# Optimization experiments

Hardware: AMD Instinct MI355X
Metric: run time of the kernel (lower is better)

The kernel has to match this reference:

```python
import jax, jax.numpy as jnp
import numpy as np
import math

B, S = 2, 2048
IN_FEATURES = 4096
OUT_FEATURES = 4096
BLOCK_SIZE = 64
NUM_FFT_MATRICES = 4
IN_BLOCKS = IN_FEATURES // BLOCK_SIZE
OUT_BLOCKS = OUT_FEATURES // BLOCK_SIZE  # 64


def setup_inputs() -> dict:
    key = jax.random.key(0)
    k1, k2 = jax.random.split(key)
    scale = 1.0 / math.sqrt(BLOCK_SIZE * IN_BLOCKS)
    x = jax.random.normal(k1, (B, S, IN_FEATURES), dtype=jnp.float32)
    circulant_params = jax.random.normal(
        k2, (NUM_FFT_MATRICES, OUT_BLOCKS, IN_BLOCKS, BLOCK_SIZE), dtype=jnp.float32) * scale
    channel_weights = jnp.ones((NUM_FFT_MATRICES,), dtype=jnp.float32) / NUM_FFT_MATRICES
    return {"x": x, "circulant_params": circulant_params, "channel_weights": channel_weights}


def reference(x, circulant_params, channel_weights):
    b, s, in_feat = x.shape
    # split channels into circulant blocks: (b, s, in_blocks, block)
    x_blocks = x.reshape(b, s, IN_BLOCKS, BLOCK_SIZE)
    x_fft = jnp.fft.rfft(x_blocks, axis=-1)                    # (b, s, i, F) complex
    circ_fft = jnp.fft.rfft(circulant_params, axis=-1)         # (m, o, i, F) complex
    # channel-weighted combine over the m fft matrices (linear, so fold into weights)
    circ_w = jnp.einsum('m,moif->oif', channel_weights.astype(circ_fft.dtype), circ_fft)
    # per-frequency complex contraction over in_blocks (the block-circulant matmul)
    y_fft = jnp.einsum('bsif,oif->bsof', x_fft, circ_w)        # (b, s, o, F)
    y = jnp.fft.irfft(y_fft, n=BLOCK_SIZE, axis=-1)            # (b, s, o, block)
    return y.reshape(b, s, OUT_FEATURES).astype(x.dtype)
```

## Files before the change

kernel.cpp:

```cpp
#include <hip/hip_runtime.h>
#include <math.h>


typedef unsigned short u16;
typedef unsigned int   u32;
typedef __attribute__((ext_vector_type(8))) short bf16x8;
typedef __attribute__((ext_vector_type(4))) float f32x4;

#define TWO_PI 6.2831853071795864769f

#define SF 2056
#define BF_ELEMS (33u*128u*128u)
#define DT_OFF   BF_ELEMS
#define DT_ELEMS (2u*4u*80u*8u)
#define E_OFF    (DT_OFF + DT_ELEMS)
#define E_ELEMS  (3u*4u*64u*8u)

__device__ __forceinline__ u16 f2bf(float f) {
    union { float f; unsigned u; } v; v.f = f;
    unsigned r = v.u + 0x7FFFu + ((v.u >> 16) & 1u);
    return (u16)(r >> 16);
}

__global__ void prep(const float* __restrict__ p, const float* __restrict__ cw,
                     u16* __restrict__ Bf, u16* __restrict__ Dt, u16* __restrict__ E) {
    const int tid = threadIdx.x;
    if (blockIdx.x == 0) {
        for (int e = tid; e < (int)DT_ELEMS; e += 256) {
            int j = e & 7, rowid = e >> 3;
            int n = rowid % 80, grp = rowid / 80;
            int k = (grp >> 2) * 32 + (grp & 3) * 8 + j;
            float v = 0.f;
            if (n < 66) {
                int f = n >> 1;
                float ang = TWO_PI * (float)((f * k) & 63) * (1.f / 64.f);
                v = (n & 1) ? -sinf(ang) : cosf(ang);
            }
            Dt[e] = f2bf(v);
        }
        for (int e = tid; e < (int)E_ELEMS; e += 256) {
            int j = e & 7, rowid = e >> 3;
            int t = rowid % 64, grp = rowid / 64;
            int k = (grp >> 2) * 32 + (grp & 3) * 8 + j;
            float v = 0.f;
            if (k < 66) {
                int f = k >> 1;
                float wf = (f == 0 || f == 32) ? 1.f : 2.f;
                float ang = TWO_PI * (float)((f * t) & 63) * (1.f / 64.f);
                v = (wf * (1.f / 64.f)) * ((k & 1) ? -sinf(ang) : cosf(ang));
            }
            E[e] = f2bf(v);
        }
        return;
    }
    __shared__ float  ct[4][64];
    __shared__ float2 trig[64];
    const int pr = tid >> 6, ln = tid & 63;
    if (tid < 64) {
        float s, c;
        sincosf(TWO_PI * (float)tid * (1.f / 64.f), &s, &c);
        trig[tid] = make_float2(s, c);
    }
    const int pg = (blockIdx.x - 1) * 4 + pr;
    const int o = pg >> 6, i = pg & 63;
    {
        const float* base = p + (size_t)o * 4096 + i * 64 + ln;
        ct[pr][ln] = cw[0] * base[0]      + cw[1] * base[262144]
                   + cw[2] * base[524288] + cw[3] * base[786432];
    }
    __syncthreads();
    if (ln < 33) {
        float cr = 0.f, ci = 0.f;
        for (int u = 0; u < 64; ++u) {
            float2 sc = trig[(ln * u) & 63];
            cr += ct[pr][u] * sc.y; ci -= ct[pr][u] * sc.x;
        }
        u16* b = Bf + (size_t)ln * 16384 + (2 * o) * 128 + 2 * i;
        b[0]   = f2bf(cr);  b[1]   = f2bf(-ci);
        b[128] = f2bf(ci);  b[129] = f2bf(cr);
    }
}

__global__ __launch_bounds__(512, 2) void fused(const float* __restrict__ x,
                                                const u16* __restrict__ Dt,
                                                const u16* __restrict__ Bf,
                                                const u16* __restrict__ E2,
                                                float* __restrict__ y) {
    __shared__ u16 sm[33 * SF];
    const int tid = threadIdx.x, lane = tid & 63, wave = tid >> 6;
    const int lm = lane & 15, q = lane >> 4, kq8 = q * 8, r0 = q * 4;
    const float* xb = x + (size_t)blockIdx.x * (16u * 4096u);

#define LOADX(XV, pass)                                                      \
    _Pragma("unroll") for (int kt = 0; kt < 2; ++kt)                         \
    _Pragma("unroll") for (int mi = 0; mi < 4; ++mi) {                       \
        const float* rp = xb + (wave*128 + (pass)*64 + mi*16 + lm)*64        \
                             + kt*32 + kq8;                                  \
        XV[kt][mi][0] = *(const float4*)rp;                                  \
        XV[kt][mi][1] = *(const float4*)(rp + 4);                            \
    }
#define MFMAPASS(XV, ACC)                                                    \
    _Pragma("unroll") for (int kt = 0; kt < 2; ++kt)                         \
    _Pragma("unroll") for (int mi = 0; mi < 4; ++mi) {                       \
        union { u16 u[8]; bf16x8 v; } pk;                                    \
        float4 p0 = XV[kt][mi][0], p1 = XV[kt][mi][1];                       \
        pk.u[0]=f2bf(p0.x); pk.u[1]=f2bf(p0.y);                              \
        pk.u[2]=f2bf(p0.z); pk.u[3]=f2bf(p0.w);                              \
        pk.u[4]=f2bf(p1.x); pk.u[5]=f2bf(p1.y);                              \
        pk.u[6]=f2bf(p1.z); pk.u[7]=f2bf(p1.w);                              \
        _Pragma("unroll") for (int ni = 0; ni < 5; ++ni)                     \
            ACC[mi][ni] = __builtin_amdgcn_mfma_f32_16x16x32_bf16(           \
                pk.v, bfr[kt][ni], ACC[mi][ni], 0, 0, 0);                    \
    }
#define SCATTER(ACC, pass)                                                   \
    {                                                                        \
        const int tok = wave*2 + (pass);                                     \
        const int sw  = (tok & 7) << 3;                                      \
        _Pragma("unroll") for (int mi = 0; mi < 4; ++mi)                     \
        _Pragma("unroll") for (int ni = 0; ni < 5; ++ni) {                   \
            const int col = ni*16 + lm;                                      \
            if (col < 66) {                                                  \
                const int f = col >> 1, par = col & 1;                       \
                f32x4 v = ACC[mi][ni];                                       \
                _Pragma("unroll") for (int r = 0; r < 4; ++r) {              \
                    int ii = mi*16 + r0 + r;                                 \
                    sm[f*SF + tok*128 + (((ii<<1)|par) ^ sw)] = f2bf(v[r]);  \
                }                                                            \
            }                                                                \
        }                                                                    \
    }
    {
        float4 xv0[2][4][2];
        LOADX(xv0, 0)
        bf16x8 bfr[2][5];
#pragma unroll
        for (int kt = 0; kt < 2; ++kt)
#pragma unroll
            for (int ni = 0; ni < 5; ++ni)
                bfr[kt][ni] = *(const bf16x8*)&Dt[((kt*4 + q)*80 + ni*16 + lm)*8];
        f32x4 acc[4][5];
#pragma unroll
        for (int mi = 0; mi < 4; ++mi)
#pragma unroll
            for (int ni = 0; ni < 5; ++ni) acc[mi][ni] = (f32x4){0.f,0.f,0.f,0.f};
        MFMAPASS(xv0, acc)
        float4 xv1[2][4][2];
        LOADX(xv1, 1)
        SCATTER(acc, 0)
#pragma unroll
        for (int mi = 0; mi < 4; ++mi)
#pragma unroll
            for (int ni = 0; ni < 5; ++ni) acc[mi][ni] = (f32x4){0.f,0.f,0.f,0.f};
        MFMAPASS(xv1, acc)
        SCATTER(acc, 1)
    }
    __syncthreads();

    bf16x8 ef[3][4];
#pragma unroll
    for (int kt = 0; kt < 3; ++kt)
#pragma unroll
        for (int mt = 0; mt < 4; ++mt)
            ef[kt][mt] = *(const bf16x8*)&E2[((kt*4 + q)*64 + mt*16 + lm)*8];

    bf16x8 af32[4], bq32[4];
#pragma unroll
    for (int ks = 0; ks < 4; ++ks)
        af32[ks] = *(const bf16x8*)&sm[32*SF + lm*128 + ((ks*32 + kq8) ^ ((lm&7)<<3))];
#pragma unroll
    for (int ks = 0; ks < 4; ++ks)
        bq32[ks] = *(const bf16x8*)&Bf[(size_t)32*16384 + (wave*16 + lm)*128 + ks*32 + kq8];
    __syncthreads();

#pragma unroll
    for (int t = 0; t < 4; ++t) {
        const int f = t*8 + wave;
        u16* sl = &sm[f * SF];
        const u16* Bff = Bf + (size_t)f * 16384;
        bf16x8 af[4];
#pragma unroll
        for (int ks = 0; ks < 4; ++ks)
            af[ks] = *(const bf16x8*)&sl[lm*128 + ((ks*32 + kq8) ^ ((lm&7)<<3))];
        bf16x8 bc[4], bn[4];
#pragma unroll
        for (int ks = 0; ks < 4; ++ks)
            bc[ks] = *(const bf16x8*)&Bff[lm*128 + ks*32 + kq8];
#pragma unroll
        for (int nt = 0; nt < 8; ++nt) {
            if (nt < 7)
#pragma unroll
                for (int ks = 0; ks < 4; ++ks)
                    bn[ks] = *(const bf16x8*)&Bff[((nt+1)*16 + lm)*128 + ks*32 + kq8];
            f32x4 c = (f32x4){0.f,0.f,0.f,0.f};
#pragma unroll
            for (int ks = 0; ks < 4; ++ks)
                c = __builtin_amdgcn_mfma_f32_16x16x32_bf16(af[ks], bc[ks], c, 0, 0, 0);
#pragma unroll
            for (int r = 0; r < 4; ++r) {
                int tok = r0 + r;
                sl[tok*128 + ((nt*16 + lm) ^ ((tok&7)<<3))] = f2bf(c[r]);
            }
#pragma unroll
            for (int ks = 0; ks < 4; ++ks) bc[ks] = bn[ks];
        }
    }
    {
        f32x4 c = (f32x4){0.f,0.f,0.f,0.f};
#pragma unroll
        for (int ks = 0; ks < 4; ++ks)
            c = __builtin_amdgcn_mfma_f32_16x16x32_bf16(af32[ks], bq32[ks], c, 0, 0, 0);
#pragma unroll
        for (int r = 0; r < 4; ++r) {
            int tok = r0 + r;
            sm[32*SF + tok*128 + ((wave*16 + lm) ^ ((tok&7)<<3))] = f2bf(c[r]);
        }
    }
    __syncthreads();

#pragma unroll
    for (int nt = 0; nt < 8; ++nt) {
        const int tokL = wave*2 + (nt >> 2);
        const int o = (nt & 3)*16 + lm;
        const int cb = tokL*128 + ((2*o) ^ ((tokL&7)<<3));
        f32x4 acc[4];
#pragma unroll
        for (int mt = 0; mt < 4; ++mt) acc[mt] = (f32x4){0.f,0.f,0.f,0.f};
#pragma unroll
        for (int kt = 0; kt < 3; ++kt) {
            union { u32 w[4]; bf16x8 v; } bq;
#pragma unroll
            for (int j = 0; j < 4; ++j) {
                int f = kt*16 + q*4 + j;
                u32 vv = 0u;
                if (f < 33) vv = *(const u32*)&sm[f*SF + cb];
                bq.w[j] = vv;
            }
#pragma unroll
            for (int mt = 0; mt < 4; ++mt)
                acc[mt] = __builtin_amdgcn_mfma_f32_16x16x32_bf16(
                    ef[kt][mt], bq.v, acc[mt], 0, 0, 0);
        }
        float* yb = y + ((size_t)(blockIdx.x*16 + tokL))*4096 + o*64;
#pragma unroll
        for (int mt = 0; mt < 4; ++mt) {
            float4 st = { acc[mt][0], acc[mt][1], acc[mt][2], acc[mt][3] };
            *(float4*)&yb[mt*16 + r0] = st;
        }
    }
}

extern "C" void kernel_launch(void* const* d_in, const int* in_sizes, int n_in,
                              void* d_out, int out_size, void* d_ws, size_t ws_size,
                              hipStream_t stream) {
    const float* x      = (const float*)d_in[0];
    const float* params = (const float*)d_in[1];
    const float* cw     = (const float*)d_in[2];
    float* out = (float*)d_out;

    u16* Bf = (u16*)d_ws;
    u16* Dt = Bf + DT_OFF;
    u16* Eg = Bf + E_OFF;

    prep<<<1025, 256, 0, stream>>>(params, cw, Bf, Dt, Eg);
    fused<<<256, 512, 0, stream>>>(x, Dt, Bf, Eg, out);
}
```

Baseline: 161.7 us.

## Split token block into two half-tiles and software-pipeline phases across them

Splits each workgroup's 16 tokens into two 8-token tiles held in separate shared-memory buffers. Phase A of the second tile and phase C of the first tile are interleaved with phase B of the other tile to overlap global loads and stores with MFMA work. The extra barriers and half-filled 16-row MFMA tiles (only q<2 rows stored) waste compute, and the shared-memory footprint stays about the same.

After: 207.9 us. 28.5% more time.

```diff
diff --git a/kernel.cpp b/kernel.cpp
--- a/kernel.cpp
+++ b/kernel.cpp
@@ -9,7 +9,8 @@
 
 #define TWO_PI 6.2831853071795864769f
 
-#define SF 2056
+#define SF 1032
+#define TILE_ELEMS (33u * SF)
 #define BF_ELEMS (33u*128u*128u)
 #define DT_OFF   BF_ELEMS
 #define DT_ELEMS (2u*4u*80u*8u)
@@ -86,20 +87,20 @@
                                                 const u16* __restrict__ Bf,
                                                 const u16* __restrict__ E2,
                                                 float* __restrict__ y) {
-    __shared__ u16 sm[33 * SF];
+    __shared__ u16 sm[2 * TILE_ELEMS];
     const int tid = threadIdx.x, lane = tid & 63, wave = tid >> 6;
     const int lm = lane & 15, q = lane >> 4, kq8 = q * 8, r0 = q * 4;
-    const float* xb = x + (size_t)blockIdx.x * (16u * 4096u);
-
-#define LOADX(XV, pass)                                                      \
+    const float* xb = x + (size_t)blockIdx.x * 65536u;
+
+#define LOADX(XV, tile)                                                      \
     _Pragma("unroll") for (int kt = 0; kt < 2; ++kt)                         \
     _Pragma("unroll") for (int mi = 0; mi < 4; ++mi) {                       \
-        const float* rp = xb + (wave*128 + (pass)*64 + mi*16 + lm)*64        \
+        const float* rp = xb + (tile)*32768 + (wave*64 + mi*16 + lm)*64      \
                              + kt*32 + kq8;                                  \
         XV[kt][mi][0] = *(const float4*)rp;                                  \
         XV[kt][mi][1] = *(const float4*)(rp + 4);                            \
     }
-#define MFMAPASS(XV, ACC)                                                    \
+#define A_MFMA(XV, ACC)                                                      \
     _Pragma("unroll") for (int kt = 0; kt < 2; ++kt)                         \
     _Pragma("unroll") for (int mi = 0; mi < 4; ++mi) {                       \
         union { u16 u[8]; bf16x8 v; } pk;                                    \
@@ -112,10 +113,8 @@
             ACC[mi][ni] = __builtin_amdgcn_mfma_f32_16x16x32_bf16(           \
                 pk.v, bfr[kt][ni], ACC[mi][ni], 0, 0, 0);                    \
     }
-#define SCATTER(ACC, pass)                                                   \
-    {                                                                        \
-        const int tok = wave*2 + (pass);                                     \
-        const int sw  = (tok & 7) << 3;                                      \
+#define SCATTER(ACC, base)                                                   \
+    {   const int sw = wave << 3;                      \
         _Pragma("unroll") for (int mi = 0; mi < 4; ++mi)                     \
         _Pragma("unroll") for (int ni = 0; ni < 5; ++ni) {                   \
             const int col = ni*16 + lm;                                      \
@@ -124,129 +123,144 @@
                 f32x4 v = ACC[mi][ni];                                       \
                 _Pragma("unroll") for (int r = 0; r < 4; ++r) {              \
                     int ii = mi*16 + r0 + r;                                 \
-                    sm[f*SF + tok*128 + (((ii<<1)|par) ^ sw)] = f2bf(v[r]);  \
+                    sm[(base) + f*SF + wave*128 + (((ii<<1)|par) ^ sw)]      \
+                        = f2bf(v[r]);                                        \
                 }                                                            \
             }                                                                \
         }                                                                    \
     }
-    {
-        float4 xv0[2][4][2];
-        LOADX(xv0, 0)
-        bf16x8 bfr[2][5];
-#pragma unroll
-        for (int kt = 0; kt < 2; ++kt)
-#pragma unroll
-            for (int ni = 0; ni < 5; ++ni)
-                bfr[kt][ni] = *(const bf16x8*)&Dt[((kt*4 + q)*80 + ni*16 + lm)*8];
-        f32x4 acc[4][5];
-#pragma unroll
-        for (int mi = 0; mi < 4; ++mi)
-#pragma unroll
-            for (int ni = 0; ni < 5; ++ni) acc[mi][ni] = (f32x4){0.f,0.f,0.f,0.f};
-        MFMAPASS(xv0, acc)
-        float4 xv1[2][4][2];
-        LOADX(xv1, 1)
-        SCATTER(acc, 0)
-#pragma unroll
-        for (int mi = 0; mi < 4; ++mi)
-#pragma unroll
-            for (int ni = 0; ni < 5; ++ni) acc[mi][ni] = (f32x4){0.f,0.f,0.f,0.f};
-        MFMAPASS(xv1, acc)
-        SCATTER(acc, 1)
-    }
-    __syncthreads();
-
+#define PHASE_B(base)                                                        \
+    _Pragma("unroll") for (int t = 0; t < 4; ++t) {                          \
+        const int f = t*8 + wave;                                            \
+        u16* sl = &sm[(base) + f * SF];                                      \
+        const u16* Bff = Bf + (size_t)f * 16384;                             \
+        bf16x8 af[4];                                                        \
+        _Pragma("unroll") for (int ks = 0; ks < 4; ++ks)                     \
+            af[ks] = *(const bf16x8*)&sl[(lm&7)*128                          \
+                                         + ((ks*32 + kq8) ^ ((lm&7)<<3))];  \
+        bf16x8 bc[4], bn[4];                                                 \
+        _Pragma("unroll") for (int ks = 0; ks < 4; ++ks)                     \
+            bc[ks] = *(const bf16x8*)&Bff[lm*128 + ks*32 + kq8];             \
+        _Pragma("unroll") for (int nt = 0; nt < 8; ++nt) {                   \
+            if (nt < 7)                                                      \
+                _Pragma("unroll") for (int ks = 0; ks < 4; ++ks)             \
+                    bn[ks] = *(const bf16x8*)&Bff[((nt+1)*16 + lm)*128       \
+                                                  + ks*32 + kq8];            \
+            f32x4 c = (f32x4){0.f,0.f,0.f,0.f};                              \
+            _Pragma("unroll") for (int ks = 0; ks < 4; ++ks)                 \
+                c = __builtin_amdgcn_mfma_f32_16x16x32_bf16(                 \
+                    af[ks], bc[ks], c, 0, 0, 0);                             \
+            if (q < 2)                                                       \
+                _Pragma("unroll") for (int r = 0; r < 4; ++r) {              \
+                    int tok = r0 + r;                                        \
+                    sl[tok*128 + ((nt*16 + lm) ^ (tok<<3))] = f2bf(c[r]);    \
+                }                                                            \
+            _Pragma("unroll") for (int ks = 0; ks < 4; ++ks) bc[ks] = bn[ks];\
+        }                                                                    \
+    }
+#define PHASE_B32(base, AF)                                                  \
+    {   f32x4 c = (f32x4){0.f,0.f,0.f,0.f};                                  \
+        _Pragma("unroll") for (int ks = 0; ks < 4; ++ks)                     \
+            c = __builtin_amdgcn_mfma_f32_16x16x32_bf16(                     \
+                AF[ks], bq32[ks], c, 0, 0, 0);                               \
+        if (q < 2)                                                           \
+            _Pragma("unroll") for (int r = 0; r < 4; ++r) {                  \
+                int tok = r0 + r;                                            \
+                sm[(base) + 32*SF + tok*128 + ((wave*16 + lm) ^ (tok<<3))]   \
+                    = f2bf(c[r]);                                            \
+            }                                                                \
+    }
+#define PHASE_C(base, tile)                                                  \
+    _Pragma("unroll") for (int nt = 0; nt < 4; ++nt) {                       \
+        const int o = nt*16 + lm;                                            \
+        const int cb = wave*128 + ((2*o) ^ (wave<<3));                       \
+        f32x4 acc[4];                                                        \
+        _Pragma("unroll") for (int mt = 0; mt < 4; ++mt)                     \
+            acc[mt] = (f32x4){0.f,0.f,0.f,0.f};                              \
+        _Pragma("unroll") for (int kt = 0; kt < 3; ++kt) {                   \
+            union { u32 w[4]; bf16x8 v; } bq;                                \
+            _Pragma("unroll") for (int j = 0; j < 4; ++j) {                  \
+                int f = kt*16 + q*4 + j;                                     \
+                u32 vv = 0u;                                                 \
+                if (f < 33) vv = *(const u32*)&sm[(base) + f*SF + cb];       \
+                bq.w[j] = vv;                                                \
+            }                                                                \
+            _Pragma("unroll") for (int mt = 0; mt < 4; ++mt)                 \
+                acc[mt] = __builtin_amdgcn_mfma_f32_16x16x32_bf16(           \
+                    ef[kt][mt], bq.v, acc[mt], 0, 0, 0);                     \
+        }                                                                    \
+        float* yb = y + ((size_t)(blockIdx.x*16 + (tile)*8 + wave))*4096     \
+                      + o*64;                                                \
+        _Pragma("unroll") for (int mt = 0; mt < 4; ++mt) {                   \
+            float4 st = { acc[mt][0], acc[mt][1], acc[mt][2], acc[mt][3] };  \
+            *(float4*)&yb[mt*16 + r0] = st;                                  \
+        }                                                                    \
+    }
+
+    bf16x8 bfr[2][5];
+#pragma unroll
+    for (int kt = 0; kt < 2; ++kt)
+#pragma unroll
+        for (int ni = 0; ni < 5; ++ni)
+            bfr[kt][ni] = *(const bf16x8*)&Dt[((kt*4 + q)*80 + ni*16 + lm)*8];
     bf16x8 ef[3][4];
 #pragma unroll
     for (int kt = 0; kt < 3; ++kt)
 #pragma unroll
         for (int mt = 0; mt < 4; ++mt)
             ef[kt][mt] = *(const bf16x8*)&E2[((kt*4 + q)*64 + mt*16 + lm)*8];
-
-    bf16x8 af32[4], bq32[4];
+    bf16x8 bq32[4];
 #pragma unroll
     for (int ks = 0; ks < 4; ++ks)
-        af32[ks] = *(const bf16x8*)&sm[32*SF + lm*128 + ((ks*32 + kq8) ^ ((lm&7)<<3))];
+        bq32[ks] = *(const bf16x8*)&Bf[(size_t)32*16384
+                                       + (wave*16 + lm)*128 + ks*32 + kq8];
+
+    {
+        float4 xv[2][4][2];
+        LOADX(xv, 0)
+        f32x4 acc[4][5];
+#pragma unroll
+        for (int mi = 0; mi < 4; ++mi)
+#pragma unroll
+            for (int ni = 0; ni < 5; ++ni) acc[mi][ni] = (f32x4){0.f,0.f,0.f,0.f};
+        A_MFMA(xv, acc)
+        SCATTER(acc, 0)
+    }
+    __syncthreads();
+    bf16x8 af32a[4];
 #pragma unroll
     for (int ks = 0; ks < 4; ++ks)
-        bq32[ks] = *(const bf16x8*)&Bf[(size_t)32*16384 + (wave*16 + lm)*128 + ks*32 + kq8];
-    __syncthreads();
-
-#pragma unroll
-    for (int t = 0; t < 4; ++t) {
-        const int f = t*8 + wave;
-        u16* sl = &sm[f * SF];
-        const u16* Bff = Bf + (size_t)f * 16384;
-        bf16x8 af[4];
-#pragma unroll
-        for (int ks = 0; ks < 4; ++ks)
-            af[ks] = *(const bf16x8*)&sl[lm*128 + ((ks*32 + kq8) ^ ((lm&7)<<3))];
-        bf16x8 bc[4], bn[4];
-#pragma unroll
-        for (int ks = 0; ks < 4; ++ks)
-            bc[ks] = *(const bf16x8*)&Bff[lm*128 + ks*32 + kq8];
-#pragma unroll
-        for (int nt = 0; nt < 8; ++nt) {
-            if (nt < 7)
-#pragma unroll
-                for (int ks = 0; ks < 4; ++ks)
-                    bn[ks] = *(const bf16x8*)&Bff[((nt+1)*16 + lm)*128 + ks*32 + kq8];
-            f32x4 c = (f32x4){0.f,0.f,0.f,0.f};
-#pragma unroll
-            for (int ks = 0; ks < 4; ++ks)
-                c = __builtin_amdgcn_mfma_f32_16x16x32_bf16(af[ks], bc[ks], c, 0, 0, 0);
-#pragma unroll
-            for (int r = 0; r < 4; ++r) {
-                int tok = r0 + r;
-                sl[tok*128 + ((nt*16 + lm) ^ ((tok&7)<<3))] = f2bf(c[r]);
-            }
-#pragma unroll
-            for (int ks = 0; ks < 4; ++ks) bc[ks] = bn[ks];
-        }
-    }
+        af32a[ks] = *(const bf16x8*)&sm[32*SF + (lm&7)*128
+                                        + ((ks*32 + kq8) ^ ((lm&7)<<3))];
+    __syncthreads();
+
+    float4 xv1[2][4][2];
+    LOADX(xv1, 1)
+    asm volatile("" ::: "memory");
+    PHASE_B(0)
+    PHASE_B32(0, af32a)
     {
-        f32x4 c = (f32x4){0.f,0.f,0.f,0.f};
-#pragma unroll
-        for (int ks = 0; ks < 4; ++ks)
-            c = __builtin_amdgcn_mfma_f32_16x16x32_bf16(af32[ks], bq32[ks], c, 0, 0, 0);
-#pragma unroll
-        for (int r = 0; r < 4; ++r) {
-            int tok = r0 + r;
-            sm[32*SF + tok*128 + ((wave*16 + lm) ^ ((tok&7)<<3))] = f2bf(c[r]);
-        }
-    }
-    __syncthreads();
-
-#pragma unroll
-    for (int nt = 0; nt < 8; ++nt) {
-        const int tokL = wave*2 + (nt >> 2);
-        const int o = (nt & 3)*16 + lm;
-        const int cb = tokL*128 + ((2*o) ^ ((tokL&7)<<3));
-        f32x4 acc[4];
-#pragma unroll
-        for (int mt = 0; mt < 4; ++mt) acc[mt] = (f32x4){0.f,0.f,0.f,0.f};
-#pragma unroll
-        for (int kt = 0; kt < 3; ++kt) {
-            union { u32 w[4]; bf16x8 v; } bq;
-#pragma unroll
-            for (int j = 0; j < 4; ++j) {
-                int f = kt*16 + q*4 + j;
-                u32 vv = 0u;
-                if (f < 33) vv = *(const u32*)&sm[f*SF + cb];
-                bq.w[j] = vv;
-            }
-#pragma unroll
-            for (int mt = 0; mt < 4; ++mt)
-                acc[mt] = __builtin_amdgcn_mfma_f32_16x16x32_bf16(
-                    ef[kt][mt], bq.v, acc[mt], 0, 0, 0);
-        }
-        float* yb = y + ((size_t)(blockIdx.x*16 + tokL))*4096 + o*64;
-#pragma unroll
-        for (int mt = 0; mt < 4; ++mt) {
-            float4 st = { acc[mt][0], acc[mt][1], acc[mt][2], acc[mt][3] };
-            *(float4*)&yb[mt*16 + r0] = st;
-        }
-    }
+        f32x4 acc[4][5];
+#pragma unroll
+        for (int mi = 0; mi < 4; ++mi)
+#pragma unroll
+            for (int ni = 0; ni < 5; ++ni) acc[mi][ni] = (f32x4){0.f,0.f,0.f,0.f};
+        A_MFMA(xv1, acc)
+        SCATTER(acc, TILE_ELEMS)
+    }
+    __syncthreads();
+    bf16x8 af32b[4];
+#pragma unroll
+    for (int ks = 0; ks < 4; ++ks)
+        af32b[ks] = *(const bf16x8*)&sm[TILE_ELEMS + 32*SF + (lm&7)*128
+                                        + ((ks*32 + kq8) ^ ((lm&7)<<3))];
+    __syncthreads();
+
+    PHASE_C(0, 0)
+    PHASE_B(TILE_ELEMS)
+    PHASE_B32(TILE_ELEMS, af32b)
+    __syncthreads();
+    PHASE_C(TILE_ELEMS, 1)
 }
 
 extern "C" void kernel_launch(void* const* d_in, const int* in_sizes, int n_in,
```
